# Kernel optimization log

Hardware: AMD Instinct MI355X
Metric: run time of the kernel (lower is better)

Reference implementation:

```python
import jax, jax.numpy as jnp
import numpy as np

K = 3        # kernel size
STRIDE = 1
PAD = 1      # k // 2


def setup_inputs() -> dict:
    key = jax.random.key(0)
    k1, k2, k3, k4 = jax.random.split(key, 4)
    B, C, H, W = 8, 128, 64, 64
    x = jax.random.normal(k1, (B, C, H, W), jnp.float32)
    offset = jax.random.normal(k2, (B, 2 * K * K, H, W), jnp.float32)
    mask = jax.random.uniform(k3, (B, K * K, H, W), jnp.float32)
    dyn_weight = jax.random.normal(k4, (B, C, K, K), jnp.float32)
    return {"x": x, "offset": offset, "mask": mask, "dyn_weight": dyn_weight}


def _deform_depthwise(img, off, msk, w):
    # img: [C,H,W], off: [2*K*K,Ho,Wo], msk: [K*K,Ho,Wo], w: [C,K,K]
    C, H, W = img.shape
    KK = K * K
    Ho = (H + 2 * PAD - K) // STRIDE + 1
    Wo = (W + 2 * PAD - K) // STRIDE + 1

    # base sampling grid per kernel tap (row-major taps, (y,x) offset pairs)
    ky, kx = jnp.meshgrid(jnp.arange(K), jnp.arange(K), indexing='ij')
    ky = ky.reshape(KK).astype(jnp.float32)
    kx = kx.reshape(KK).astype(jnp.float32)
    base_y = (jnp.arange(Ho) * STRIDE - PAD).astype(jnp.float32)
    base_x = (jnp.arange(Wo) * STRIDE - PAD).astype(jnp.float32)
    off = off.reshape(KK, 2, Ho, Wo)
    py = base_y[None, :, None] + ky[:, None, None] + off[:, 0]   # [KK,Ho,Wo]
    px = base_x[None, None, :] + kx[:, None, None] + off[:, 1]   # [KK,Ho,Wo]

    y0f = jnp.floor(py)
    x0f = jnp.floor(px)
    dy = py - y0f
    dx = px - x0f

    def gather(yf, xf):
        # zero-padded bilinear corner gather -> [C,KK,Ho,Wo]
        valid = (yf >= 0) & (yf < H) & (xf >= 0) & (xf < W)
        yi = jnp.clip(yf, 0, H - 1).astype(jnp.int32)
        xi = jnp.clip(xf, 0, W - 1).astype(jnp.int32)
        return img[:, yi, xi] * valid.astype(img.dtype)[None]

    v00 = gather(y0f, x0f)
    v01 = gather(y0f, x0f + 1)
    v10 = gather(y0f + 1, x0f)
    v11 = gather(y0f + 1, x0f + 1)

    sampled = (v00 * ((1 - dy) * (1 - dx))[None] + v01 * ((1 - dy) * dx)[None]
               + v10 * (dy * (1 - dx))[None] + v11 * (dy * dx)[None])
    modulated = sampled * msk[None]                               # [C,KK,Ho,Wo]
    return jnp.einsum('ckhw,ck->chw', modulated, w.reshape(C, KK))


def reference(x, offset, mask, dyn_weight):
    # dyn_weight path: per-sample depthwise modulated deformable conv
    # (weight [C,1,K,K] with groups=C, no bias), vmapped over batch instead
    # of the original Python loop.
    return jax.vmap(_deform_depthwise)(x, offset, mask, dyn_weight)
```

## Files before the change

kernel.cpp:

```cpp
#include <hip/hip_runtime.h>


#define BB 8
#define CC 128
#define HH 64
#define WW 64
#define HWs (HH*WW)
#define KKT 9
#define CH 16
#define NCG (CC/CH)
#define CPI 4
#define NIT (CH/CPI)
#define ROWS 4
#define NHS (HH/ROWS)
#define WLO 6
#define WR  (ROWS+14)
#define CLO 6
#define WC  76
#define CELLS (WR*WC)
#define NTHR 256
#define NK  ((CELLS + NTHR - 1)/NTHR)

__global__ __launch_bounds__(NTHR, 2)
void mdcn_kernel(const float* __restrict__ x,
                 const float* __restrict__ offset,
                 const float* __restrict__ mask,
                 const float* __restrict__ dynw,
                 float* __restrict__ out)
{
    __shared__ float4 lds[CELLS];

    const int blk = blockIdx.x;
    const int hs = blk & (NHS - 1);
    const int cg = (blk >> 4) & (NCG - 1);
    const int b  = blk >> 7;
    const int tid = threadIdx.x;
    const int w = tid & 63;
    const int h0 = hs * ROWS;
    const int h = h0 + (tid >> 6);

    const float* xg = x + (size_t)(b * CC + cg * CH) * HWs;

    float4 stg[NK];
    #define STAGE_LOAD(XP)                                                    \
    do {                                                                      \
        const float* xp_ = (XP);                                              \
        _Pragma("unroll")                                                     \
        for (int k = 0; k < NK; ++k) {                                        \
            const int idx = tid + k * NTHR;                                   \
            float4 v = make_float4(0.f, 0.f, 0.f, 0.f);                       \
            if (idx < CELLS) {                                                \
                const int row = idx / WC;                                     \
                const int col = idx - row * WC - CLO;                         \
                const int ar  = h0 - WLO + row;                               \
                if ((unsigned)ar < (unsigned)HH &&                            \
                    (unsigned)col < (unsigned)WW) {                           \
                    const float* pp = xp_ + ar * WW + col;                    \
                    v.x = pp[0 * HWs]; v.y = pp[1 * HWs];                     \
                    v.z = pp[2 * HWs]; v.w = pp[3 * HWs];                     \
                }                                                             \
            }                                                                 \
            stg[k] = v;                                                       \
        }                                                                     \
    } while (0)

    #define STAGE_WRITE()                                                     \
    do {                                                                      \
        _Pragma("unroll")                                                     \
        for (int k = 0; k < NK; ++k) {                                        \
            const int idx = tid + k * NTHR;                                   \
            if (idx < CELLS) lds[idx] = stg[k];                               \
        }                                                                     \
    } while (0)

    STAGE_LOAD(xg);

    float mv[KKT], dyv[KKT], dxv[KKT];
    int   woff[KKT];
    int   badmask = 0;
    const float* offp = offset + (size_t)b * (2 * KKT) * HWs + h * WW + w;
    const float* mskp = mask   + (size_t)b * KKT * HWs       + h * WW + w;
    #pragma unroll
    for (int t = 0; t < KKT; ++t) {
        const float oy = offp[(2 * t)     * HWs];
        const float ox = offp[(2 * t + 1) * HWs];
        const float m  = mskp[t * HWs];
        const float py = (float)(h - 1 + t / 3) + oy;
        const float px = (float)(w - 1 + t % 3) + ox;
        const float fy = floorf(py), fx = floorf(px);
        const int y0 = (int)fy, x0 = (int)fx;
        dyv[t] = py - fy;
        dxv[t] = px - fx;
        const bool inwin = (y0 >= h0 - WLO) && (y0 <= h0 - WLO + WR - 2) &&
                           (x0 >= -CLO)     && (x0 <= -CLO + WC - 2);
        if (!inwin) {
            badmask |= (1 << t);
            woff[t] = 0;
            mv[t] = 0.f;
        } else {
            woff[t] = (y0 - (h0 - WLO)) * WC + (x0 + CLO);
            mv[t] = m;
        }
    }
    const int anybad = __any(badmask != 0);

    STAGE_WRITE();
    __syncthreads();

    const float* wtb  = dynw + (size_t)(b * CC + cg * CH) * KKT;
    float*       outp = out  + (size_t)(b * CC + cg * CH) * HWs + h * WW + w;

    for (int it = 0; it < NIT; ++it) {
        const float* wt = wtb + it * CPI * KKT;
        float s0 = 0.f, s1 = 0.f, s2 = 0.f, s3 = 0.f;

        if (anybad) {
            #pragma unroll
            for (int t = 0; t < KKT; ++t) {
                if (badmask & (1 << t)) {
                    const float oy = offp[(2 * t)     * HWs];
                    const float ox = offp[(2 * t + 1) * HWs];
                    const float m  = mskp[t * HWs];
                    const float py = (float)(h - 1 + t / 3) + oy;
                    const float px = (float)(w - 1 + t % 3) + ox;
                    const float fy = floorf(py), fx = floorf(px);
                    const float dy = py - fy, dx = px - fx;
                    const int y0 = (int)fy, x0 = (int)fx;
                    const int y1 = y0 + 1,  x1 = x0 + 1;
                    const int cy0 = min(max(y0, 0), HH - 1);
                    const int cy1 = min(max(y1, 0), HH - 1);
                    const int cx0 = min(max(x0, 0), WW - 1);
                    const int cx1 = min(max(x1, 0), WW - 1);
                    const float m00 = ((unsigned)y0 < HH && (unsigned)x0 < WW) ? 1.f : 0.f;
                    const float m01 = ((unsigned)y0 < HH && (unsigned)x1 < WW) ? 1.f : 0.f;
                    const float m10 = ((unsigned)y1 < HH && (unsigned)x0 < WW) ? 1.f : 0.f;
                    const float m11 = ((unsigned)y1 < HH && (unsigned)x1 < WW) ? 1.f : 0.f;
                    const float omdy = 1.f - dy, omdx = 1.f - dx;
                    #pragma unroll
                    for (int c = 0; c < CPI; ++c) {
                        const float* pl = xg + (size_t)(it * CPI + c) * HWs;
                        const float v = pl[cy0 * WW + cx0] * m00 * (omdy * omdx)
                                      + pl[cy0 * WW + cx1] * m01 * (omdy * dx)
                                      + pl[cy1 * WW + cx0] * m10 * (dy * omdx)
                                      + pl[cy1 * WW + cx1] * m11 * (dy * dx);
                        const float add = v * m * wt[c * KKT + t];
                        if      (c == 0) s0 += add;
                        else if (c == 1) s1 += add;
                        else if (c == 2) s2 += add;
                        else             s3 += add;
                    }
                }
            }
        }

        if (it + 1 < NIT) {
            STAGE_LOAD(xg + (size_t)(it + 1) * CPI * HWs);
        }

        #pragma unroll
        for (int t = 0; t < KKT; ++t) {
            const float4 c00 = lds[woff[t]];
            const float4 c01 = lds[woff[t] + 1];
            const float4 c10 = lds[woff[t] + WC];
            const float4 c11 = lds[woff[t] + WC + 1];
            const float dy = dyv[t], dx = dxv[t], m = mv[t];
            const float omdy = 1.f - dy, omdx = 1.f - dx;
            const float w00 = omdy * omdx * m, w01 = omdy * dx * m;
            const float w10 = dy * omdx * m,   w11 = dy * dx * m;
            const float v0 = c00.x * w00 + c01.x * w01 + c10.x * w10 + c11.x * w11;
            const float v1 = c00.y * w00 + c01.y * w01 + c10.y * w10 + c11.y * w11;
            const float v2 = c00.z * w00 + c01.z * w01 + c10.z * w10 + c11.z * w11;
            const float v3 = c00.w * w00 + c01.w * w01 + c10.w * w10 + c11.w * w11;
            s0 += v0 * wt[0 * KKT + t];
            s1 += v1 * wt[1 * KKT + t];
            s2 += v2 * wt[2 * KKT + t];
            s3 += v3 * wt[3 * KKT + t];
        }

        outp[(size_t)(it * CPI + 0) * HWs] = s0;
        outp[(size_t)(it * CPI + 1) * HWs] = s1;
        outp[(size_t)(it * CPI + 2) * HWs] = s2;
        outp[(size_t)(it * CPI + 3) * HWs] = s3;

        if (it + 1 < NIT) {
            __syncthreads();
            STAGE_WRITE();
            __syncthreads();
        }
    }
    #undef STAGE_LOAD
    #undef STAGE_WRITE
}

extern "C" void kernel_launch(void* const* d_in, const int* in_sizes, int n_in,
                              void* d_out, int out_size, void* d_ws, size_t ws_size,
                              hipStream_t stream) {
    const float* x      = (const float*)d_in[0];
    const float* offset = (const float*)d_in[1];
    const float* mask   = (const float*)d_in[2];
    const float* dynw   = (const float*)d_in[3];
    float* out = (float*)d_out;

    dim3 grid(BB * NCG * NHS);
    dim3 block(NTHR);
    mdcn_kernel<<<grid, block, 0, stream>>>(x, offset, mask, dynw, out);
}
```

Measured before the change: 35.66 us.

## Process four channels per block and shrink the LDS halo window

Reduces channels per block from 16 to 4, removing the inner channel-chunk loop and its double-buffered staging and barriers, so the grid grows fourfold. The block index is reordered so channel groups vary fastest, letting neighbouring blocks share offset/mask reads in cache. The LDS halo window shrinks from 6 to 5 cells, which frees shared memory for more resident blocks but sends more taps to the slow global fallback path. Offset and mask loads and the bilinear setup are now repeated per 4 channels instead of per 16, raising redundant global traffic.

```diff
diff --git a/kernel.cpp b/kernel.cpp
--- a/kernel.cpp
+++ b/kernel.cpp
@@ -7,16 +7,14 @@
 #define WW 64
 #define HWs (HH*WW)
 #define KKT 9
-#define CH 16
+#define CH 4
 #define NCG (CC/CH)
-#define CPI 4
-#define NIT (CH/CPI)
 #define ROWS 4
 #define NHS (HH/ROWS)
-#define WLO 6
-#define WR  (ROWS+14)
-#define CLO 6
-#define WC  76
+#define WLO 5
+#define WR  (ROWS+12)
+#define CLO 5
+#define WC  74
 #define CELLS (WR*WC)
 #define NTHR 256
 #define NK  ((CELLS + NTHR - 1)/NTHR)
@@ -31,9 +29,10 @@
     __shared__ float4 lds[CELLS];
 
     const int blk = blockIdx.x;
-    const int hs = blk & (NHS - 1);
-    const int cg = (blk >> 4) & (NCG - 1);
-    const int b  = blk >> 7;
+    const int cg = blk & (NCG - 1);
+    const int r  = blk >> 5;
+    const int hs = r & (NHS - 1);
+    const int b  = r >> 4;
     const int tid = threadIdx.x;
     const int w = tid & 63;
     const int h0 = hs * ROWS;
@@ -42,38 +41,22 @@
     const float* xg = x + (size_t)(b * CC + cg * CH) * HWs;
 
     float4 stg[NK];
-    #define STAGE_LOAD(XP)                                                    \
-    do {                                                                      \
-        const float* xp_ = (XP);                                              \
-        _Pragma("unroll")                                                     \
-        for (int k = 0; k < NK; ++k) {                                        \
-            const int idx = tid + k * NTHR;                                   \
-            float4 v = make_float4(0.f, 0.f, 0.f, 0.f);                       \
-            if (idx < CELLS) {                                                \
-                const int row = idx / WC;                                     \
-                const int col = idx - row * WC - CLO;                         \
-                const int ar  = h0 - WLO + row;                               \
-                if ((unsigned)ar < (unsigned)HH &&                            \
-                    (unsigned)col < (unsigned)WW) {                           \
-                    const float* pp = xp_ + ar * WW + col;                    \
-                    v.x = pp[0 * HWs]; v.y = pp[1 * HWs];                     \
-                    v.z = pp[2 * HWs]; v.w = pp[3 * HWs];                     \
-                }                                                             \
-            }                                                                 \
-            stg[k] = v;                                                       \
-        }                                                                     \
-    } while (0)
-
-    #define STAGE_WRITE()                                                     \
-    do {                                                                      \
-        _Pragma("unroll")                                                     \
-        for (int k = 0; k < NK; ++k) {                                        \
-            const int idx = tid + k * NTHR;                                   \
-            if (idx < CELLS) lds[idx] = stg[k];                               \
-        }                                                                     \
-    } while (0)
-
-    STAGE_LOAD(xg);
+    #pragma unroll
+    for (int k = 0; k < NK; ++k) {
+        const int idx = tid + k * NTHR;
+        float4 v = make_float4(0.f, 0.f, 0.f, 0.f);
+        if (idx < CELLS) {
+            const int row = idx / WC;
+            const int col = idx - row * WC - CLO;
+            const int ar  = h0 - WLO + row;
+            if ((unsigned)ar < (unsigned)HH && (unsigned)col < (unsigned)WW) {
+                const float* pp = xg + ar * WW + col;
+                v.x = pp[0 * HWs]; v.y = pp[1 * HWs];
+                v.z = pp[2 * HWs]; v.w = pp[3 * HWs];
+            }
+        }
+        stg[k] = v;
+    }
 
     float mv[KKT], dyv[KKT], dxv[KKT];
     int   woff[KKT];
@@ -104,92 +87,81 @@
     }
     const int anybad = __any(badmask != 0);
 
-    STAGE_WRITE();
-    __syncthreads();
-
-    const float* wtb  = dynw + (size_t)(b * CC + cg * CH) * KKT;
+    const float* wt   = dynw + (size_t)(b * CC + cg * CH) * KKT;
     float*       outp = out  + (size_t)(b * CC + cg * CH) * HWs + h * WW + w;
 
-    for (int it = 0; it < NIT; ++it) {
-        const float* wt = wtb + it * CPI * KKT;
-        float s0 = 0.f, s1 = 0.f, s2 = 0.f, s3 = 0.f;
+    float s0 = 0.f, s1 = 0.f, s2 = 0.f, s3 = 0.f;
 
-        if (anybad) {
-            #pragma unroll
-            for (int t = 0; t < KKT; ++t) {
-                if (badmask & (1 << t)) {
-                    const float oy = offp[(2 * t)     * HWs];
-                    const float ox = offp[(2 * t + 1) * HWs];
-                    const float m  = mskp[t * HWs];
-                    const float py = (float)(h - 1 + t / 3) + oy;
-                    const float px = (float)(w - 1 + t % 3) + ox;
-                    const float fy = floorf(py), fx = floorf(px);
-                    const float dy = py - fy, dx = px - fx;
-                    const int y0 = (int)fy, x0 = (int)fx;
-                    const int y1 = y0 + 1,  x1 = x0 + 1;
-                    const int cy0 = min(max(y0, 0), HH - 1);
-                    const int cy1 = min(max(y1, 0), HH - 1);
-                    const int cx0 = min(max(x0, 0), WW - 1);
-                    const int cx1 = min(max(x1, 0), WW - 1);
-                    const float m00 = ((unsigned)y0 < HH && (unsigned)x0 < WW) ? 1.f : 0.f;
-                    const float m01 = ((unsigned)y0 < HH && (unsigned)x1 < WW) ? 1.f : 0.f;
-                    const float m10 = ((unsigned)y1 < HH && (unsigned)x0 < WW) ? 1.f : 0.f;
-                    const float m11 = ((unsigned)y1 < HH && (unsigned)x1 < WW) ? 1.f : 0.f;
-                    const float omdy = 1.f - dy, omdx = 1.f - dx;
-                    #pragma unroll
-                    for (int c = 0; c < CPI; ++c) {
-                        const float* pl = xg + (size_t)(it * CPI + c) * HWs;
-                        const float v = pl[cy0 * WW + cx0] * m00 * (omdy * omdx)
-                                      + pl[cy0 * WW + cx1] * m01 * (omdy * dx)
-                                      + pl[cy1 * WW + cx0] * m10 * (dy * omdx)
-                                      + pl[cy1 * WW + cx1] * m11 * (dy * dx);
-                        const float add = v * m * wt[c * KKT + t];
-                        if      (c == 0) s0 += add;
-                        else if (c == 1) s1 += add;
-                        else if (c == 2) s2 += add;
-                        else             s3 += add;
-                    }
+    if (anybad) {
+        #pragma unroll
+        for (int t = 0; t < KKT; ++t) {
+            if (badmask & (1 << t)) {
+                const float oy = offp[(2 * t)     * HWs];
+                const float ox = offp[(2 * t + 1) * HWs];
+                const float m  = mskp[t * HWs];
+                const float py = (float)(h - 1 + t / 3) + oy;
+                const float px = (float)(w - 1 + t % 3) + ox;
+                const float fy = floorf(py), fx = floorf(px);
+                const float dy = py - fy, dx = px - fx;
+                const int y0 = (int)fy, x0 = (int)fx;
+                const int y1 = y0 + 1,  x1 = x0 + 1;
+                const int cy0 = min(max(y0, 0), HH - 1);
+                const int cy1 = min(max(y1, 0), HH - 1);
+                const int cx0 = min(max(x0, 0), WW - 1);
+                const int cx1 = min(max(x1, 0), WW - 1);
+                const float m00 = ((unsigned)y0 < HH && (unsigned)x0 < WW) ? 1.f : 0.f;
+                const float m01 = ((unsigned)y0 < HH && (unsigned)x1 < WW) ? 1.f : 0.f;
+                const float m10 = ((unsigned)y1 < HH && (unsigned)x0 < WW) ? 1.f : 0.f;
+                const float m11 = ((unsigned)y1 < HH && (unsigned)x1 < WW) ? 1.f : 0.f;
+                const float omdy = 1.f - dy, omdx = 1.f - dx;
+                #pragma unroll
+                for (int c = 0; c < CH; ++c) {
+                    const float* pl = xg + (size_t)c * HWs;
+                    const float v = pl[cy0 * WW + cx0] * m00 * (omdy * omdx)
+                                  + pl[cy0 * WW + cx1] * m01 * (omdy * dx)
+                                  + pl[cy1 * WW + cx0] * m10 * (dy * omdx)
+                                  + pl[cy1 * WW + cx1] * m11 * (dy * dx);
+                    const float add = v * m * wt[c * KKT + t];
+                    if      (c == 0) s0 += add;
+                    else if (c == 1) s1 += add;
+                    else if (c == 2) s2 += add;
+                    else             s3 += add;
                 }
             }
         }
+    }
 
-        if (it + 1 < NIT) {
-            STAGE_LOAD(xg + (size_t)(it + 1) * CPI * HWs);
-        }
+    #pragma unroll
+    for (int k = 0; k < NK; ++k) {
+        const int idx = tid + k * NTHR;
+        if (idx < CELLS) lds[idx] = stg[k];
+    }
+    __syncthreads();
 
-        #pragma unroll
-        for (int t = 0; t < KKT; ++t) {
-            const float4 c00 = lds[woff[t]];
-            const float4 c01 = lds[woff[t] + 1];
-            const float4 c10 = lds[woff[t] + WC];
-            const float4 c11 = lds[woff[t] + WC + 1];
-            const float dy = dyv[t], dx = dxv[t], m = mv[t];
-            const float omdy = 1.f - dy, omdx = 1.f - dx;
-            const float w00 = omdy * omdx * m, w01 = omdy * dx * m;
-            const float w10 = dy * omdx * m,   w11 = dy * dx * m;
-            const float v0 = c00.x * w00 + c01.x * w01 + c10.x * w10 + c11.x * w11;
-            const float v1 = c00.y * w00 + c01.y * w01 + c10.y * w10 + c11.y * w11;
-            const float v2 = c00.z * w00 + c01.z * w01 + c10.z * w10 + c11.z * w11;
-            const float v3 = c00.w * w00 + c01.w * w01 + c10.w * w10 + c11.w * w11;
-            s0 += v0 * wt[0 * KKT + t];
-            s1 += v1 * wt[1 * KKT + t];
-            s2 += v2 * wt[2 * KKT + t];
-            s3 += v3 * wt[3 * KKT + t];
-        }
+    #pragma unroll
+    for (int t = 0; t < KKT; ++t) {
+        const float4 c00 = lds[woff[t]];
+        const float4 c01 = lds[woff[t] + 1];
+        const float4 c10 = lds[woff[t] + WC];
+        const float4 c11 = lds[woff[t] + WC + 1];
+        const float dy = dyv[t], dx = dxv[t], m = mv[t];
+        const float omdy = 1.f - dy, omdx = 1.f - dx;
+        const float w00 = omdy * omdx * m, w01 = omdy * dx * m;
+        const float w10 = dy * omdx * m,   w11 = dy * dx * m;
+        const float v0 = c00.x * w00 + c01.x * w01 + c10.x * w10 + c11.x * w11;
+        const float v1 = c00.y * w00 + c01.y * w01 + c10.y * w10 + c11.y * w11;
+        const float v2 = c00.z * w00 + c01.z * w01 + c10.z * w10 + c11.z * w11;
+        const float v3 = c00.w * w00 + c01.w * w01 + c10.w * w10 + c11.w * w11;
+        s0 += v0 * wt[0 * KKT + t];
+        s1 += v1 * wt[1 * KKT + t];
+        s2 += v2 * wt[2 * KKT + t];
+        s3 += v3 * wt[3 * KKT + t];
+    }
 
-        outp[(size_t)(it * CPI + 0) * HWs] = s0;
-        outp[(size_t)(it * CPI + 1) * HWs] = s1;
-        outp[(size_t)(it * CPI + 2) * HWs] = s2;
-        outp[(size_t)(it * CPI + 3) * HWs] = s3;
-
-        if (it + 1 < NIT) {
-            __syncthreads();
-            STAGE_WRITE();
-            __syncthreads();
-        }
-    }
-    #undef STAGE_LOAD
-    #undef STAGE_WRITE
+    outp[0 * HWs] = s0;
+    outp[1 * HWs] = s1;
+    outp[2 * HWs] = s2;
+    outp[3 * HWs] = s3;
 }
 
 extern "C" void kernel_launch(void* const* d_in, const int* in_sizes, int n_in,
```

New measurement: 38.42 us. 7.8% more time.
